# Kernel tuning notes

Measured on AMD Instinct MI355X. Metric: run time of the kernel, lower is better.

The kernel has to match this reference:

```python
import jax, jax.numpy as jnp
import numpy as np

B, S, D_IN = 16, 2048, 8
H = 512
WIN = 10
D = D_IN + 1  # time-augmented path dim
SIG_DIM = D + D * D + D * D * D  # depth-3 signature channels = 819


def setup_inputs() -> dict:
    key = jax.random.key(0)
    ks = jax.random.split(key, 5)
    s = 1.0 / np.sqrt(H)
    return {
        "x": jax.random.normal(ks[0], (B, S, D_IN), jnp.float32),
        "W_ih": jax.random.uniform(ks[1], (4 * H, D_IN + SIG_DIM), jnp.float32, -s, s),
        "W_hh": jax.random.uniform(ks[2], (4 * H, H), jnp.float32, -s, s),
        "b_ih": jax.random.uniform(ks[3], (4 * H,), jnp.float32, -s, s),
        "b_hh": jax.random.uniform(ks[4], (4 * H,), jnp.float32, -s, s),
    }


def _windowed_signatures(x):
    # x: (B, S, D_IN). Returns per-step depth-3 signatures of the trailing
    # window of the time-augmented path, with a zero basepoint prepended.
    b, s, _ = x.shape
    time = jnp.linspace(0.0, 1.0, s, dtype=x.dtype)
    xt = jnp.concatenate(
        [x, jnp.broadcast_to(time[None, :, None], (b, s, 1))], axis=-1
    )  # (B,S,D)
    # Window indices clipped at 0: repeated points give zero increments, which
    # leave the signature unchanged (exp(0)=Id). This exactly reproduces the
    # short-window and t=0 duplicated-path cases of the torch module.
    idx = jnp.clip(
        jnp.arange(s)[:, None] - (WIN - 1) + jnp.arange(WIN)[None, :], 0, s - 1
    )
    win = xt[:, idx, :]
    # Zero basepoint -> first increment is the first window point itself.
    incs = jnp.concatenate([win[:, :, :1, :], jnp.diff(win, axis=2)], axis=2)
    incs = jnp.moveaxis(incs, 2, 0)

    def chen_step(carry, dx):
        # Chen's identity: S <- S (tensor) exp(dx), truncated at depth 3.
        s1, s2, s3 = carry
        e2 = 0.5 * dx[..., :, None] * dx[..., None, :]
        e3 = (dx[..., :, None, None] * dx[..., None, :, None] * dx[..., None, None, :]) / 6.0
        n3 = (s3
              + s2[..., :, :, None] * dx[..., None, None, :]
              + s1[..., :, None, None] * e2[..., None, :, :]
              + e3)
        n2 = s2 + s1[..., :, None] * dx[..., None, :] + e2
        n1 = s1 + dx
        return (n1, n2, n3), None

    z1 = jnp.zeros((b, s, D), x.dtype)
    z2 = jnp.zeros((b, s, D, D), x.dtype)
    z3 = jnp.zeros((b, s, D, D, D), x.dtype)
    (s1, s2, s3), _ = jax.lax.scan(chen_step, (z1, z2, z3), incs)
    return jnp.concatenate(
        [s1, s2.reshape(b, s, D * D), s3.reshape(b, s, D * D * D)], axis=-1
    )  # (B, S, SIG_DIM), level-major lexicographic order as in signatory


def reference(x, W_ih, W_hh, b_ih, b_hh):
    b = x.shape[0]
    sigs = _windowed_signatures(x)
    x_aug = jnp.concatenate([x, sigs], axis=-1)  # (B, S, D_IN + SIG_DIM)
    bias = b_ih + b_hh

    def lstm_step(carry, xt):
        h, c = carry
        g = xt @ W_ih.T + h @ W_hh.T + bias
        i, f, gg, o = jnp.split(g, 4, axis=-1)  # torch gate order i,f,g,o
        c = jax.nn.sigmoid(f) * c + jax.nn.sigmoid(i) * jnp.tanh(gg)
        h = jax.nn.sigmoid(o) * jnp.tanh(c)
        return (h, c), h

    h0 = jnp.zeros((b, H), x.dtype)
    (hn, cn), ys = jax.lax.scan(lstm_step, (h0, h0), jnp.swapaxes(x_aug, 0, 1))
    return jnp.swapaxes(ys, 0, 1), hn, cn
```

## Files before the change

### kernel.cpp

```cpp
#include <hip/hip_runtime.h>
#include <hip/hip_bf16.h>
#include <stdint.h>

typedef short bf16x8 __attribute__((ext_vector_type(8)));
typedef float f32x4 __attribute__((ext_vector_type(4)));

#define B_ 16
#define S_ 2048
#define H_ 512
#define NG 2048
#define KA 827
#define KP 832
#define NPOS (B_*S_)

#define OFF_XAUG 0
#define OFF_WIHB 54525952
#define OFF_G    57933824
#define OFF_RING 0
#define RING_U64_PER_SLOT 2048
#define SENT32 0x7F807F80u
#define SENT64 0x7F807F807F807F80ull

__device__ __forceinline__ unsigned short f2bf(float f){
  union { float f; unsigned u; } v; v.f = f;
  unsigned u = v.u;
  unsigned r = (u + 0x7FFFu + ((u >> 16) & 1u)) >> 16;
  return (unsigned short)r;
}
__device__ __forceinline__ float bf2f(unsigned short s){
  union { unsigned u; float f; } v; v.u = ((unsigned)s) << 16;
  return v.f;
}
__device__ __forceinline__ float sigf(float x){ return 1.0f / (1.0f + __expf(-x)); }
__device__ __forceinline__ float tanhfast(float x){ return 1.0f - 2.0f / (__expf(2.0f*x) + 1.0f); }

__global__ __launch_bounds__(256) void sigk(const float* __restrict__ x,
                                            unsigned short* __restrict__ xaug){
  const int bid = blockIdx.x;
  const int s = bid >> 4, b = bid & 15;
  const int tid = threadIdx.x;
  __shared__ float win[10][9];
  __shared__ float s1b[2][9];
  __shared__ float s2b[2][81];
  if (tid < 90){
    int w = tid / 9, d = tid - w*9;
    int idx = s - 9 + w; if (idx < 0) idx = 0;
    win[w][d] = (d < 8) ? x[((size_t)b*S_ + idx)*8 + d] : (float)idx * (1.0f/2047.0f);
  }
  if (tid < 81) s2b[0][tid] = 0.0f;
  if (tid < 9)  s1b[0][tid] = 0.0f;
  __syncthreads();
  const int i0 = tid / 81;
  const int jj = (tid / 9) % 9;
  const int kk = tid % 9;
  float r0 = 0.0f, r1 = 0.0f, r2 = 0.0f;
  int p = 0;
  for (int w = 0; w < 10; ++w){
    if (tid < 243){
      float dj  = win[w][jj]   - (w ? win[w-1][jj]   : 0.0f);
      float dk  = win[w][kk]   - (w ? win[w-1][kk]   : 0.0f);
      float di0 = win[w][i0]   - (w ? win[w-1][i0]   : 0.0f);
      float di1 = win[w][i0+3] - (w ? win[w-1][i0+3] : 0.0f);
      float di2 = win[w][i0+6] - (w ? win[w-1][i0+6] : 0.0f);
      float e2 = 0.5f * dj * dk;
      float e3 = dj * dk * (1.0f/6.0f);
      r0 += s2b[p][i0*9+jj]*dk     + s1b[p][i0]*e2   + di0*e3;
      r1 += s2b[p][(i0+3)*9+jj]*dk + s1b[p][i0+3]*e2 + di1*e3;
      r2 += s2b[p][(i0+6)*9+jj]*dk + s1b[p][i0+6]*e2 + di2*e3;
    }
    if (tid < 81){
      int si = tid / 9, sj = tid - si*9;
      float dsi = win[w][si] - (w ? win[w-1][si] : 0.0f);
      float dsj = win[w][sj] - (w ? win[w-1][sj] : 0.0f);
      s2b[p^1][tid] = s2b[p][tid] + s1b[p][si]*dsj + 0.5f*dsi*dsj;
    }
    if (tid < 9){
      float dt = win[w][tid] - (w ? win[w-1][tid] : 0.0f);
      s1b[p^1][tid] = s1b[p][tid] + dt;
    }
    __syncthreads();
    p ^= 1;
  }
  unsigned short* row = xaug + (size_t)bid * KP;
  if (tid < 8)  row[tid]      = f2bf(x[((size_t)b*S_ + s)*8 + tid]);
  if (tid < 9)  row[8 + tid]  = f2bf(s1b[p][tid]);
  if (tid < 81) row[17 + tid] = f2bf(s2b[p][tid]);
  if (tid < 243){
    row[98 + tid]       = f2bf(r0);
    row[98 + tid + 243] = f2bf(r1);
    row[98 + tid + 486] = f2bf(r2);
  }
  if (tid < KP - KA) row[KA + tid] = 0;
}

__global__ void convk(const float* __restrict__ W, unsigned short* __restrict__ o){
  int idx = blockIdx.x*256 + threadIdx.x;
  if (idx >= NG*KP) return;
  int n = idx / KP, k = idx - n*KP;
  o[idx] = (k < KA) ? f2bf(W[(size_t)n*KA + k]) : (unsigned short)0;
}

__global__ __launch_bounds__(256) void gemmk(const unsigned short* __restrict__ A,
                                             const unsigned short* __restrict__ Bw,
                                             unsigned short* __restrict__ G){
  __shared__ unsigned short as[128][40];
  __shared__ unsigned short bs[128][40];
  const int tid = threadIdx.x;
  const int l = tid & 63, w = tid >> 6;
  const int wr = w >> 1, wc = w & 1;
  const int M0 = blockIdx.x * 128, N0 = blockIdx.y * 128;
  f32x4 acc[4][4];
  for (int i=0;i<4;i++) for (int j2=0;j2<4;j2++) acc[i][j2] = (f32x4){0,0,0,0};
  const int lrow = l & 15, kq8 = (l >> 4) * 8;
  for (int kt = 0; kt < 26; ++kt){
    const int kbase = kt * 32;
    for (int c = tid; c < 512; c += 256){
      int row = c >> 2, kc = (c & 3) * 8;
      uint4 va = *(const uint4*)(A  + (size_t)(M0 + row)*KP + kbase + kc);
      *(uint4*)(&as[row][kc]) = va;
      uint4 vb = *(const uint4*)(Bw + (size_t)(N0 + row)*KP + kbase + kc);
      *(uint4*)(&bs[row][kc]) = vb;
    }
    __syncthreads();
    bf16x8 af[4], bfv[4];
    for (int i=0;i<4;i++)    af[i]  = *(const bf16x8*)(&as[wr*64 + i*16 + lrow][kq8]);
    for (int j2=0;j2<4;j2++) bfv[j2] = *(const bf16x8*)(&bs[wc*64 + j2*16 + lrow][kq8]);
    for (int i=0;i<4;i++)
      for (int j2=0;j2<4;j2++)
        acc[i][j2] = __builtin_amdgcn_mfma_f32_16x16x32_bf16(af[i], bfv[j2], acc[i][j2], 0, 0, 0);
    __syncthreads();
  }
  const int rq = (l >> 4) * 4;
  for (int i=0;i<4;i++){
    for (int q=0;q<4;q++){
      int grow_ = M0 + wr*64 + i*16 + rq + q;
      unsigned short* gout = G + (size_t)grow_*NG + N0 + wc*64 + lrow;
      for (int j2=0;j2<4;j2++)
        gout[j2*16] = f2bf(acc[i][j2][q]);
    }
  }
}

__global__ __launch_bounds__(256) void sentk(uint4* __restrict__ ring){
  const size_t i = (size_t)blockIdx.x*256 + threadIdx.x;
  uint4 s; s.x = SENT32; s.y = SENT32; s.z = SENT32; s.w = SENT32;
  #pragma unroll
  for (int k = 0; k < 8; ++k)
    ring[i + (size_t)k*262144] = s;
}

__global__ __launch_bounds__(64, 1) void recurk(const float* __restrict__ Whh,
    const float* __restrict__ bih, const float* __restrict__ bhh,
    const unsigned short* __restrict__ G, float* __restrict__ out,
    unsigned long long* __restrict__ ring){
  const int W = ((blockIdx.x & 7) << 3) | (blockIdx.x >> 3);
  const int l = threadIdx.x;
  const int b = l & 15, kq = l >> 4;
  const int hbase = W * 8;

  bf16x8 a0[16], a1[16];
  {
    const int p = l & 15;
    const int arow0 = (p < 8) ? (hbase + p) : (512 + hbase + (p - 8));
    const int arow1 = arow0 + 1024;
    const float* w0 = Whh + (size_t)arow0 * H_;
    const float* w1 = Whh + (size_t)arow1 * H_;
    for (int kk2 = 0; kk2 < 16; ++kk2){
      const int k0 = kk2*32 + kq*8;
      float4 v0 = *(const float4*)(w0 + k0);
      float4 v1 = *(const float4*)(w0 + k0 + 4);
      bf16x8 av;
      av[0]=(short)f2bf(v0.x); av[1]=(short)f2bf(v0.y); av[2]=(short)f2bf(v0.z); av[3]=(short)f2bf(v0.w);
      av[4]=(short)f2bf(v1.x); av[5]=(short)f2bf(v1.y); av[6]=(short)f2bf(v1.z); av[7]=(short)f2bf(v1.w);
      a0[kk2] = av;
      float4 u0 = *(const float4*)(w1 + k0);
      float4 u1 = *(const float4*)(w1 + k0 + 4);
      bf16x8 bv2;
      bv2[0]=(short)f2bf(u0.x); bv2[1]=(short)f2bf(u0.y); bv2[2]=(short)f2bf(u0.z); bv2[3]=(short)f2bf(u0.w);
      bv2[4]=(short)f2bf(u1.x); bv2[5]=(short)f2bf(u1.y); bv2[6]=(short)f2bf(u1.z); bv2[7]=(short)f2bf(u1.w);
      a1[kk2] = bv2;
    }
  }
  const int col0 = ((kq < 2) ? (kq*4) : (512 + (kq-2)*4)) + hbase;
  const int col1 = col0 + 1024;
  float bias0[4], bias1[4];
  #pragma unroll
  for (int q=0;q<4;q++){
    bias0[q] = bih[col0+q] + bhh[col0+q];
    bias1[q] = bih[col1+q] + bhh[col1+q];
  }
  const bool low = (kq < 2);
  const int hcol = hbase + (low ? kq*4 : (kq-2)*4);
  const size_t ownw = (size_t)W*32 + b*2 + kq;
  float cr[4] = {0,0,0,0};

  for (int t = 0; t < S_; ++t){
    const unsigned short* gp = G + ((size_t)t*16 + b) * NG;
    const short4 g0 = *(const short4*)(gp + col0);
    const short4 g1 = *(const short4*)(gp + col1);

    f32x4 acc0 = (f32x4){0,0,0,0}, acc0b = (f32x4){0,0,0,0};
    f32x4 acc1 = (f32x4){0,0,0,0}, acc1b = (f32x4){0,0,0,0};
    if (t){
      const unsigned long long* sp = ring + (size_t)(t-1)*RING_U64_PER_SLOT;
      unsigned long long rv[32];
      for (;;){
        #pragma unroll
        for (int i = 0; i < 16; ++i){
          const size_t wi = (size_t)((i*4 + kq)*32 + b*2);
          rv[2*i]   = __hip_atomic_load(sp + wi,     __ATOMIC_RELAXED, __HIP_MEMORY_SCOPE_AGENT);
          rv[2*i+1] = __hip_atomic_load(sp + wi + 1, __ATOMIC_RELAXED, __HIP_MEMORY_SCOPE_AGENT);
        }
        unsigned ok = 1;
        #pragma unroll
        for (int i = 0; i < 32; ++i) ok &= (rv[i] != SENT64);
        if (__all((int)ok)) break;
      }
      #pragma unroll
      for (int i = 0; i < 8; ++i){
        uint2 lo0 = __builtin_bit_cast(uint2, rv[4*i]);
        uint2 hi0 = __builtin_bit_cast(uint2, rv[4*i+1]);
        uint4 u0v; u0v.x = lo0.x; u0v.y = lo0.y; u0v.z = hi0.x; u0v.w = hi0.y;
        bf16x8 bv0 = __builtin_bit_cast(bf16x8, u0v);
        acc0  = __builtin_amdgcn_mfma_f32_16x16x32_bf16(a0[2*i],   bv0, acc0,  0, 0, 0);
        acc1  = __builtin_amdgcn_mfma_f32_16x16x32_bf16(a1[2*i],   bv0, acc1,  0, 0, 0);
        uint2 lo1 = __builtin_bit_cast(uint2, rv[4*i+2]);
        uint2 hi1 = __builtin_bit_cast(uint2, rv[4*i+3]);
        uint4 u1v; u1v.x = lo1.x; u1v.y = lo1.y; u1v.z = hi1.x; u1v.w = hi1.y;
        bf16x8 bv1 = __builtin_bit_cast(bf16x8, u1v);
        acc0b = __builtin_amdgcn_mfma_f32_16x16x32_bf16(a0[2*i+1], bv1, acc0b, 0, 0, 0);
        acc1b = __builtin_amdgcn_mfma_f32_16x16x32_bf16(a1[2*i+1], bv1, acc1b, 0, 0, 0);
      }
    }
    float ga0[4] = { bf2f((unsigned short)g0.x), bf2f((unsigned short)g0.y),
                     bf2f((unsigned short)g0.z), bf2f((unsigned short)g0.w) };
    float ga1[4] = { bf2f((unsigned short)g1.x), bf2f((unsigned short)g1.y),
                     bf2f((unsigned short)g1.z), bf2f((unsigned short)g1.w) };
    float own0[4], own1[4], oth0[4], oth1[4];
    #pragma unroll
    for (int q=0;q<4;q++){
      own0[q] = (acc0[q] + acc0b[q]) + ga0[q] + bias0[q];
      own1[q] = (acc1[q] + acc1b[q]) + ga1[q] + bias1[q];
    }
    #pragma unroll
    for (int q=0;q<4;q++){
      oth0[q] = __shfl_xor(own0[q], 32, 64);
      oth1[q] = __shfl_xor(own1[q], 32, 64);
    }
    float h4[4];
    #pragma unroll
    for (int q=0;q<4;q++){
      float iv = low ? own0[q] : oth0[q];
      float fv = low ? oth0[q] : own0[q];
      float gv = low ? own1[q] : oth1[q];
      float ov = low ? oth1[q] : own1[q];
      cr[q] = sigf(fv)*cr[q] + sigf(iv)*tanhfast(gv);
      h4[q] = sigf(ov)*tanhfast(cr[q]);
    }
    if (low){
      if (t < S_ - 1){
        unsigned long long pk = (unsigned long long)f2bf(h4[0])
                              | ((unsigned long long)f2bf(h4[1]) << 16)
                              | ((unsigned long long)f2bf(h4[2]) << 32)
                              | ((unsigned long long)f2bf(h4[3]) << 48);
        __hip_atomic_exchange(ring + (size_t)t*RING_U64_PER_SLOT + ownw,
                              pk, __ATOMIC_RELAXED, __HIP_MEMORY_SCOPE_AGENT);
      }
      f32x4 hw4; hw4[0]=h4[0]; hw4[1]=h4[1]; hw4[2]=h4[2]; hw4[3]=h4[3];
      __builtin_nontemporal_store(hw4, (f32x4*)(out + ((size_t)b*S_ + t)*H_ + hcol));
      if (t == S_ - 1){
        float* hn = out + (size_t)B_*S_*H_;
        float* cn = hn + B_*H_;
        #pragma unroll
        for (int q=0;q<4;q++){
          hn[b*H_ + hcol + q] = h4[q];
          cn[b*H_ + hcol + q] = cr[q];
        }
      }
    }
  }
}

extern "C" void kernel_launch(void* const* d_in, const int* in_sizes, int n_in,
                              void* d_out, int out_size, void* d_ws, size_t ws_size,
                              hipStream_t stream){
  const float* x   = (const float*)d_in[0];
  const float* Wih = (const float*)d_in[1];
  const float* Whh = (const float*)d_in[2];
  const float* bih = (const float*)d_in[3];
  const float* bhh = (const float*)d_in[4];
  float* out = (float*)d_out;
  char* ws = (char*)d_ws;
  unsigned short* xaug     = (unsigned short*)(ws + OFF_XAUG);
  unsigned short* wihb     = (unsigned short*)(ws + OFF_WIHB);
  unsigned short* G        = (unsigned short*)(ws + OFF_G);
  unsigned long long* ring = (unsigned long long*)(ws + OFF_RING);

  sigk<<<NPOS, 256, 0, stream>>>(x, xaug);
  convk<<<(NG*KP + 255)/256, 256, 0, stream>>>(Wih, wihb);
  gemmk<<<dim3(256, 16), 256, 0, stream>>>(xaug, wihb, G);
  sentk<<<1024, 256, 0, stream>>>((uint4*)(ws + OFF_RING));
  recurk<<<64, 64, 0, stream>>>(Whh, bih, bhh, G, out, ring);
}
```

Measured before the change: 4.930 ms.

## Consume ring slices incrementally and defer fp32 output writes to separate kernel

After: 10.20 ms. 107% more time.

```diff
diff --git a/kernel.cpp b/kernel.cpp
--- a/kernel.cpp
+++ b/kernel.cpp
@@ -204,33 +204,53 @@
     if (t){
       const unsigned long long* sp = ring + (size_t)(t-1)*RING_U64_PER_SLOT;
       unsigned long long rv[32];
-      for (;;){
+      #pragma unroll
+      for (int i = 0; i < 16; ++i){
+        const size_t wi = (size_t)((i*4 + kq)*32 + b*2);
+        rv[2*i]   = __hip_atomic_load(sp + wi,     __ATOMIC_RELAXED, __HIP_MEMORY_SCOPE_AGENT);
+        rv[2*i+1] = __hip_atomic_load(sp + wi + 1, __ATOMIC_RELAXED, __HIP_MEMORY_SCOPE_AGENT);
+      }
+      unsigned done = 0;
+      do {
+        unsigned newly = 0;
         #pragma unroll
         for (int i = 0; i < 16; ++i){
-          const size_t wi = (size_t)((i*4 + kq)*32 + b*2);
-          rv[2*i]   = __hip_atomic_load(sp + wi,     __ATOMIC_RELAXED, __HIP_MEMORY_SCOPE_AGENT);
-          rv[2*i+1] = __hip_atomic_load(sp + wi + 1, __ATOMIC_RELAXED, __HIP_MEMORY_SCOPE_AGENT);
+          if (!(done & (1u << i))){
+            int ok = (rv[2*i] != SENT64) & (rv[2*i+1] != SENT64);
+            if (__all(ok)) newly |= (1u << i);
+          }
         }
-        unsigned ok = 1;
+        const unsigned pend = 0xFFFFu & ~(done | newly);
+        if (pend){
+          #pragma unroll
+          for (int i = 0; i < 16; ++i){
+            if (pend & (1u << i)){
+              const size_t wi = (size_t)((i*4 + kq)*32 + b*2);
+              if (rv[2*i]   == SENT64)
+                rv[2*i]   = __hip_atomic_load(sp + wi,     __ATOMIC_RELAXED, __HIP_MEMORY_SCOPE_AGENT);
+              if (rv[2*i+1] == SENT64)
+                rv[2*i+1] = __hip_atomic_load(sp + wi + 1, __ATOMIC_RELAXED, __HIP_MEMORY_SCOPE_AGENT);
+            }
+          }
+        }
         #pragma unroll
-        for (int i = 0; i < 32; ++i) ok &= (rv[i] != SENT64);
-        if (__all((int)ok)) break;
-      }
-      #pragma unroll
-      for (int i = 0; i < 8; ++i){
-        uint2 lo0 = __builtin_bit_cast(uint2, rv[4*i]);
-        uint2 hi0 = __builtin_bit_cast(uint2, rv[4*i+1]);
-        uint4 u0v; u0v.x = lo0.x; u0v.y = lo0.y; u0v.z = hi0.x; u0v.w = hi0.y;
-        bf16x8 bv0 = __builtin_bit_cast(bf16x8, u0v);
-        acc0  = __builtin_amdgcn_mfma_f32_16x16x32_bf16(a0[2*i],   bv0, acc0,  0, 0, 0);
-        acc1  = __builtin_amdgcn_mfma_f32_16x16x32_bf16(a1[2*i],   bv0, acc1,  0, 0, 0);
-        uint2 lo1 = __builtin_bit_cast(uint2, rv[4*i+2]);
-        uint2 hi1 = __builtin_bit_cast(uint2, rv[4*i+3]);
-        uint4 u1v; u1v.x = lo1.x; u1v.y = lo1.y; u1v.z = hi1.x; u1v.w = hi1.y;
-        bf16x8 bv1 = __builtin_bit_cast(bf16x8, u1v);
-        acc0b = __builtin_amdgcn_mfma_f32_16x16x32_bf16(a0[2*i+1], bv1, acc0b, 0, 0, 0);
-        acc1b = __builtin_amdgcn_mfma_f32_16x16x32_bf16(a1[2*i+1], bv1, acc1b, 0, 0, 0);
-      }
+        for (int i = 0; i < 16; ++i){
+          if (newly & (1u << i)){
+            uint2 lo = __builtin_bit_cast(uint2, rv[2*i]);
+            uint2 hi = __builtin_bit_cast(uint2, rv[2*i+1]);
+            uint4 u; u.x = lo.x; u.y = lo.y; u.z = hi.x; u.w = hi.y;
+            bf16x8 bv = __builtin_bit_cast(bf16x8, u);
+            if (i & 1){
+              acc0b = __builtin_amdgcn_mfma_f32_16x16x32_bf16(a0[i], bv, acc0b, 0, 0, 0);
+              acc1b = __builtin_amdgcn_mfma_f32_16x16x32_bf16(a1[i], bv, acc1b, 0, 0, 0);
+            } else {
+              acc0  = __builtin_amdgcn_mfma_f32_16x16x32_bf16(a0[i], bv, acc0,  0, 0, 0);
+              acc1  = __builtin_amdgcn_mfma_f32_16x16x32_bf16(a1[i], bv, acc1,  0, 0, 0);
+            }
+          }
+        }
+        done |= newly;
+      } while (done != 0xFFFFu);
     }
     float ga0[4] = { bf2f((unsigned short)g0.x), bf2f((unsigned short)g0.y),
                      bf2f((unsigned short)g0.z), bf2f((unsigned short)g0.w) };
@@ -258,16 +278,12 @@
       h4[q] = sigf(ov)*tanhfast(cr[q]);
     }
     if (low){
-      if (t < S_ - 1){
-        unsigned long long pk = (unsigned long long)f2bf(h4[0])
-                              | ((unsigned long long)f2bf(h4[1]) << 16)
-                              | ((unsigned long long)f2bf(h4[2]) << 32)
-                              | ((unsigned long long)f2bf(h4[3]) << 48);
-        __hip_atomic_exchange(ring + (size_t)t*RING_U64_PER_SLOT + ownw,
-                              pk, __ATOMIC_RELAXED, __HIP_MEMORY_SCOPE_AGENT);
-      }
-      f32x4 hw4; hw4[0]=h4[0]; hw4[1]=h4[1]; hw4[2]=h4[2]; hw4[3]=h4[3];
-      __builtin_nontemporal_store(hw4, (f32x4*)(out + ((size_t)b*S_ + t)*H_ + hcol));
+      unsigned long long pk = (unsigned long long)f2bf(h4[0])
+                            | ((unsigned long long)f2bf(h4[1]) << 16)
+                            | ((unsigned long long)f2bf(h4[2]) << 32)
+                            | ((unsigned long long)f2bf(h4[3]) << 48);
+      __hip_atomic_exchange(ring + (size_t)t*RING_U64_PER_SLOT + ownw,
+                            pk, __ATOMIC_RELAXED, __HIP_MEMORY_SCOPE_AGENT);
       if (t == S_ - 1){
         float* hn = out + (size_t)B_*S_*H_;
         float* cn = hn + B_*H_;
@@ -279,6 +295,25 @@
       }
     }
   }
+}
+
+__global__ __launch_bounds__(256) void outk(const unsigned long long* __restrict__ ring,
+                                            float* __restrict__ out){
+  const size_t idx = (size_t)blockIdx.x*256 + threadIdx.x;
+  const int w = (int)(idx & 127);
+  const size_t bt = idx >> 7;
+  const int t = (int)(bt & 2047);
+  const int b = (int)(bt >> 11);
+  const int hcol = w * 4;
+  const int W = hcol >> 3;
+  const int kq = (hcol >> 2) & 1;
+  unsigned long long v = ring[(size_t)t*RING_U64_PER_SLOT + (size_t)W*32 + b*2 + kq];
+  float4 o;
+  o.x = bf2f((unsigned short)(v));
+  o.y = bf2f((unsigned short)(v >> 16));
+  o.z = bf2f((unsigned short)(v >> 32));
+  o.w = bf2f((unsigned short)(v >> 48));
+  *(float4*)(out + ((size_t)b*S_ + t)*H_ + hcol) = o;
 }
 
 extern "C" void kernel_launch(void* const* d_in, const int* in_sizes, int n_in,
@@ -301,4 +336,5 @@
   gemmk<<<dim3(256, 16), 256, 0, stream>>>(xaug, wihb, G);
   sentk<<<1024, 256, 0, stream>>>((uint4*)(ws + OFF_RING));
   recurk<<<64, 64, 0, stream>>>(Whh, bih, bhh, G, out, ring);
-}
+  outk<<<16384, 256, 0, stream>>>(ring, out);
+}
```
